# Optimization experiments

Hardware: AMD Instinct MI355X
Metric: run time of the kernel (lower is better)

Reference implementation:

```python
import jax, jax.numpy as jnp
import numpy as np

N_NODES = 50000
N_EDGES = 1_600_000
IN_DIM = 64
HID_DIM = 64
OUT_DIM = 64


def setup_inputs() -> dict:
    key = jax.random.key(0)
    k = jax.random.split(key, 7)
    feat = jax.random.normal(k[0], (N_NODES, IN_DIM), dtype=jnp.float32)
    src = jax.random.randint(k[1], (N_EDGES,), 0, N_NODES, dtype=jnp.int32)
    dst = jax.random.randint(k[2], (N_EDGES,), 0, N_NODES, dtype=jnp.int32)
    # nn.init.normal_(weight, std=0.1); bias default uniform ~ small, use 0.1*randn
    W1 = 0.1 * jax.random.normal(k[3], (HID_DIM, IN_DIM), dtype=jnp.float32)
    b1 = 0.1 * jax.random.normal(k[4], (HID_DIM,), dtype=jnp.float32)
    W2 = 0.1 * jax.random.normal(k[5], (OUT_DIM, HID_DIM), dtype=jnp.float32)
    b2 = 0.1 * jax.random.normal(k[6], (OUT_DIM,), dtype=jnp.float32)
    return {"feat": feat, "src": src, "dst": dst, "W1": W1, "b1": b1, "W2": W2, "b2": b2}


def _gnn_layer(h, src, dst, W, b):
    # copy_u + sum: gather source-node features along edges, scatter-sum to dst
    agg = jax.ops.segment_sum(h[src], dst, num_segments=N_NODES)  # [N, d_in]
    return agg @ W.T + b  # nn.Linear


def reference(feat, src, dst, W1, b1, W2, b2):
    h = _gnn_layer(feat, src, dst, W1, b1)
    h = jnp.tanh(h)
    h = _gnn_layer(h, src, dst, W2, b2)
    return h
```

## Files before the change

### kernel.cpp

```cpp
#include <hip/hip_runtime.h>

#define N_NODES 50000
#define N_EDGES 1600000
#define DIM 64
#define NBK 196
#define BIN_BLOCKS 391
#define CSR_CAP 12288
#define OCT_CAP 1536
#define BCAP 13312
#define G1_BLOCKS 391
#define NB_AGG8 6250

__device__ __forceinline__ unsigned short f2bf(float f) {
    union { float f; unsigned u; } v; v.f = f;
    unsigned r = v.u + 0x7FFF + ((v.u >> 16) & 1);
    return (unsigned short)(r >> 16);
}
__device__ __forceinline__ float bf2f(unsigned short h) {
    union { unsigned u; float f; } v; v.u = ((unsigned)h) << 16;  return v.f;
}
__device__ __forceinline__ float blo(unsigned u) {
    union { unsigned u; float f; } v; v.u = u << 16; return v.f;
}
__device__ __forceinline__ float bhi(unsigned u) {
    union { unsigned u; float f; } v; v.u = u & 0xFFFF0000u; return v.f;
}

__global__ __launch_bounds__(512) void bin_edges(const int* __restrict__ src,
                                                 const int* __restrict__ dst,
                                                 int* __restrict__ bcur,
                                                 int* __restrict__ binned) {
    __shared__ int cnt[256];
    __shared__ int lofs[256];
    __shared__ int shiftv[256];
    __shared__ uint2 stag2[4096];
    int tid = threadIdx.x;

    if (tid < 256) cnt[tid] = 0;
    __syncthreads();

    int base = blockIdx.x * 4096;
    int oct = blockIdx.x & 7;
    int nedge = N_EDGES - base;
    if (nedge > 4096) nedge = 4096;

    int sreg[8], dreg[8];
#pragma unroll
    for (int i = 0; i < 8; ++i) {
        int e = base + i * 512 + tid;
        if (e < N_EDGES) { sreg[i] = src[e]; dreg[i] = dst[e]; }
        else             { sreg[i] = 0;      dreg[i] = -1; }
    }
    int myr[8];
#pragma unroll
    for (int i = 0; i < 8; ++i)
        if (dreg[i] >= 0) myr[i] = atomicAdd(&cnt[dreg[i] >> 8], 1);
    __syncthreads();

    if (tid < 64) {
        int c0 = cnt[tid * 4 + 0];
        int c1 = cnt[tid * 4 + 1];
        int c2 = cnt[tid * 4 + 2];
        int c3 = cnt[tid * 4 + 3];
        int t = c0 + c1 + c2 + c3;
        int p = t;
#pragma unroll
        for (int off = 1; off < 64; off <<= 1) {
            int u = __shfl_up(p, off);
            if (tid >= off) p += u;
        }
        int ex = p - t;
        int b0 = tid * 4;
        lofs[b0 + 0] = ex;
        lofs[b0 + 1] = ex + c0;
        lofs[b0 + 2] = ex + c0 + c1;
        lofs[b0 + 3] = ex + c0 + c1 + c2;
        if (b0 + 0 < NBK && c0) shiftv[b0 + 0] = (b0 + 0) * CSR_CAP + oct * OCT_CAP
            + atomicAdd(&bcur[((b0 + 0) * 8 + oct) * 16], c0) - lofs[b0 + 0];
        if (b0 + 1 < NBK && c1) shiftv[b0 + 1] = (b0 + 1) * CSR_CAP + oct * OCT_CAP
            + atomicAdd(&bcur[((b0 + 1) * 8 + oct) * 16], c1) - lofs[b0 + 1];
        if (b0 + 2 < NBK && c2) shiftv[b0 + 2] = (b0 + 2) * CSR_CAP + oct * OCT_CAP
            + atomicAdd(&bcur[((b0 + 2) * 8 + oct) * 16], c2) - lofs[b0 + 2];
        if (b0 + 3 < NBK && c3) shiftv[b0 + 3] = (b0 + 3) * CSR_CAP + oct * OCT_CAP
            + atomicAdd(&bcur[((b0 + 3) * 8 + oct) * 16], c3) - lofs[b0 + 3];
    }
    __syncthreads();

#pragma unroll
    for (int i = 0; i < 8; ++i) {
        if (dreg[i] >= 0) {
            int b = dreg[i] >> 8;
            uint2 rec;
            rec.x = (unsigned)(((dreg[i] & 255) << 16) | sreg[i]);
            rec.y = (unsigned)b;
            stag2[lofs[b] + myr[i]] = rec;
        }
    }
    __syncthreads();

    for (int i = tid; i < nedge; i += 512) {
        uint2 v = stag2[i];
        binned[i + shiftv[v.y]] = (int)v.x;
    }
}

__global__ __launch_bounds__(256) void csr_gemm1(const int* __restrict__ binned,
                                                 const int* __restrict__ bcur,
                                                 unsigned* __restrict__ nodeinfo,
                                                 unsigned short* __restrict__ csr16,
                                                 const float* __restrict__ X,
                                                 const float* __restrict__ W,
                                                 unsigned short* __restrict__ T) {
    __shared__ __align__(16) char smem[32768];
    int tid = threadIdx.x;

    if (blockIdx.x >= NBK) {
        float4* xs = (float4*)smem;
        int w = tid >> 6, lane = tid & 63;
        int nbase = (blockIdx.x - NBK) * 128;

        float4 wreg[16];
        const float4* wp = (const float4*)(W + lane * 64);
#pragma unroll
        for (int k4 = 0; k4 < 16; ++k4) wreg[k4] = wp[k4];

        const float4* xg = (const float4*)X;
        for (int L = tid; L < 2048; L += 256) {
            int row = nbase + (L >> 4);
            float4 v = {0.f, 0.f, 0.f, 0.f};
            if (row < N_NODES) v = xg[(size_t)row * 16 + (L & 15)];
            xs[L] = v;
        }
        __syncthreads();

        for (int g = 0; g < 8; ++g) {
            int n0 = w * 32 + g * 4;
            float accA = 0.f, accB = 0.f, accC = 0.f, accD = 0.f;
#pragma unroll
            for (int k4 = 0; k4 < 16; ++k4) {
                float4 w4 = wreg[k4];
                float4 xA = xs[(n0 + 0) * 16 + k4];
                float4 xB = xs[(n0 + 1) * 16 + k4];
                float4 xC = xs[(n0 + 2) * 16 + k4];
                float4 xD = xs[(n0 + 3) * 16 + k4];
                accA += xA.x * w4.x + xA.y * w4.y + xA.z * w4.z + xA.w * w4.w;
                accB += xB.x * w4.x + xB.y * w4.y + xB.z * w4.z + xB.w * w4.w;
                accC += xC.x * w4.x + xC.y * w4.y + xC.z * w4.z + xC.w * w4.w;
                accD += xD.x * w4.x + xD.y * w4.y + xD.z * w4.z + xD.w * w4.w;
            }
            int gn = nbase + n0;
            unsigned short vA = (gn + 0 == N_NODES) ? (unsigned short)0 : f2bf(accA);
            unsigned short vB = (gn + 1 == N_NODES) ? (unsigned short)0 : f2bf(accB);
            unsigned short vC = (gn + 2 == N_NODES) ? (unsigned short)0 : f2bf(accC);
            unsigned short vD = (gn + 3 == N_NODES) ? (unsigned short)0 : f2bf(accD);
            if (gn + 0 <= N_NODES) T[(size_t)(gn + 0) * 64 + lane] = vA;
            if (gn + 1 <= N_NODES) T[(size_t)(gn + 1) * 64 + lane] = vB;
            if (gn + 2 <= N_NODES) T[(size_t)(gn + 2) * 64 + lane] = vC;
            if (gn + 3 <= N_NODES) T[(size_t)(gn + 3) * 64 + lane] = vD;
        }
        return;
    }

    int* cnt  = (int*)smem;
    int* cnt2 = cnt + 256;
    int* ofs  = cnt2 + 256;
    int* sb   = ofs + 256;
    int* mo   = sb + 256;
    int b = blockIdx.x;
    int bbase = b * BCAP;
    cnt[tid] = 0; cnt2[tid] = 0;
    if (tid < 8) {
        int m = bcur[(b * 8 + tid) * 16];
        mo[tid] = m > OCT_CAP ? OCT_CAP : m;
    }
    __syncthreads();

    for (int oct = 0; oct < 8; ++oct) {
        const int* ib = binned + b * CSR_CAP + oct * OCT_CAP;
        int m = mo[oct];
        int i = tid;
        for (; i + 768 < m; i += 1024) {
            int p0 = ib[i], p1 = ib[i + 256], p2 = ib[i + 512], p3 = ib[i + 768];
            atomicAdd(&cnt[(p0 >> 16) & 255], 1);
            atomicAdd(&cnt[(p1 >> 16) & 255], 1);
            atomicAdd(&cnt[(p2 >> 16) & 255], 1);
            atomicAdd(&cnt[(p3 >> 16) & 255], 1);
        }
        for (; i < m; i += 256)
            atomicAdd(&cnt[(ib[i] >> 16) & 255], 1);
    }
    __syncthreads();

    int myc = cnt[tid];
    int v = (myc + 15) & ~15;
    sb[tid] = v;
    __syncthreads();
    for (int off = 1; off < 256; off <<= 1) {
        int u = (tid >= off) ? sb[tid - off] : 0;
        __syncthreads();
        sb[tid] += u;
        __syncthreads();
    }
    int o = sb[tid] - v;
    ofs[tid] = o;
    int node = (b << 8) + tid;
    if (node < N_NODES)
        nodeinfo[node] = ((unsigned)v << 23) | (unsigned)(bbase + o);
    for (int i = myc; i < v; ++i)
        csr16[bbase + o + i] = (unsigned short)N_NODES;
    __syncthreads();

    for (int oct = 0; oct < 8; ++oct) {
        const int* ib = binned + b * CSR_CAP + oct * OCT_CAP;
        int m = mo[oct];
        int i = tid;
        for (; i + 768 < m; i += 1024) {
            int p0 = ib[i], p1 = ib[i + 256], p2 = ib[i + 512], p3 = ib[i + 768];
            int d0 = (p0 >> 16) & 255, d1 = (p1 >> 16) & 255;
            int d2 = (p2 >> 16) & 255, d3 = (p3 >> 16) & 255;
            int r0 = atomicAdd(&cnt2[d0], 1);
            int r1 = atomicAdd(&cnt2[d1], 1);
            int r2 = atomicAdd(&cnt2[d2], 1);
            int r3 = atomicAdd(&cnt2[d3], 1);
            csr16[bbase + ofs[d0] + r0] = (unsigned short)(p0 & 0xFFFF);
            csr16[bbase + ofs[d1] + r1] = (unsigned short)(p1 & 0xFFFF);
            csr16[bbase + ofs[d2] + r2] = (unsigned short)(p2 & 0xFFFF);
            csr16[bbase + ofs[d3] + r3] = (unsigned short)(p3 & 0xFFFF);
        }
        for (; i < m; i += 256) {
            int p = ib[i];
            int dl = (p >> 16) & 255;
            int r = atomicAdd(&cnt2[dl], 1);
            csr16[bbase + ofs[dl] + r] = (unsigned short)(p & 0xFFFF);
        }
    }
}

#define ACC8(d)                                                     \
    a0 += blo(d.x); a1 += bhi(d.x); a2 += blo(d.y); a3 += bhi(d.y); \
    a4 += blo(d.z); a5 += bhi(d.z); a6 += blo(d.w); a7 += bhi(d.w);

__global__ __launch_bounds__(512) void agg_fuse1(const unsigned short* __restrict__ T,
                                                 const unsigned short* __restrict__ csr,
                                                 const unsigned* __restrict__ nodeinfo,
                                                 const float* __restrict__ b1,
                                                 const float* __restrict__ W2,
                                                 unsigned short* __restrict__ T2) {
    __shared__ __align__(16) float4 W2t4[1024];
    __shared__ __align__(16) float part[8][8][72];
    int tid = threadIdx.x;
    int w = tid >> 6;
    int lane = tid & 63;
    int g8 = lane >> 3;
    int fs = lane & 7;
    int node = blockIdx.x * 8 + w;

    for (int L4 = tid; L4 < 1024; L4 += 512) {
        int k4 = L4 >> 6, f = L4 & 63;
        W2t4[L4] = *(const float4*)(W2 + f * 64 + k4 * 4);
    }

    unsigned info = nodeinfo[node];
    float bias = b1[lane];
    int pos = (int)(info & 0x7FFFFFu);
    int nch = (int)(info >> 23) >> 3;
    const unsigned short* ip = csr + pos + g8;
    const uint4* Tp = (const uint4*)T;
    float a0 = 0.f, a1 = 0.f, a2 = 0.f, a3 = 0.f, a4 = 0.f, a5 = 0.f, a6 = 0.f, a7 = 0.f;
    int c = 0;
    for (; c + 4 <= nch; c += 4) {
        int j0 = ip[c * 8];
        int j1 = ip[c * 8 + 8];
        int j2 = ip[c * 8 + 16];
        int j3 = ip[c * 8 + 24];
        uint4 d0 = Tp[j0 * 8 + fs];
        uint4 d1 = Tp[j1 * 8 + fs];
        uint4 d2 = Tp[j2 * 8 + fs];
        uint4 d3 = Tp[j3 * 8 + fs];
        ACC8(d0) ACC8(d1) ACC8(d2) ACC8(d3)
    }
    if (c < nch) {
        int j0 = ip[c * 8];
        int j1 = ip[c * 8 + 8];
        uint4 d0 = Tp[j0 * 8 + fs];
        uint4 d1 = Tp[j1 * 8 + fs];
        ACC8(d0) ACC8(d1)
    }
    float4 pa = {a0, a1, a2, a3};
    float4 pb = {a4, a5, a6, a7};
    *(float4*)&part[w][g8][fs * 8] = pa;
    *(float4*)&part[w][g8][fs * 8 + 4] = pb;
    __syncthreads();

    float acc = bias;
#pragma unroll
    for (int g = 0; g < 8; ++g) acc += part[w][g][lane];

    float e = __expf(2.f * acc);
    part[w][0][lane] = 1.f - 2.f / (e + 1.f);

    const float* hrow = &part[w][0][0];
    float tf = 0.f;
#pragma unroll
    for (int k4 = 0; k4 < 16; ++k4) {
        float4 hv = *(const float4*)(hrow + k4 * 4);
        float4 wv = W2t4[k4 * 64 + lane];
        tf += hv.x * wv.x + hv.y * wv.y + hv.z * wv.z + hv.w * wv.w;
    }
    T2[(size_t)node * DIM + lane] = f2bf(tf);

    if (blockIdx.x == 0 && tid < 64)
        T2[(size_t)N_NODES * DIM + tid] = 0;
}

__global__ __launch_bounds__(512) void agg_out(const unsigned short* __restrict__ T,
                                               const unsigned short* __restrict__ csr,
                                               const unsigned* __restrict__ nodeinfo,
                                               const float* __restrict__ bias,
                                               float* __restrict__ outp) {
    __shared__ __align__(16) float part[8][8][72];
    int tid = threadIdx.x;
    int w = tid >> 6;
    int lane = tid & 63;
    int g8 = lane >> 3;
    int fs = lane & 7;
    int node = blockIdx.x * 8 + w;

    unsigned info = nodeinfo[node];
    float bv = bias[lane];
    int pos = (int)(info & 0x7FFFFFu);
    int nch = (int)(info >> 23) >> 3;
    const unsigned short* ip = csr + pos + g8;
    const uint4* Tp = (const uint4*)T;
    float a0 = 0.f, a1 = 0.f, a2 = 0.f, a3 = 0.f, a4 = 0.f, a5 = 0.f, a6 = 0.f, a7 = 0.f;
    int c = 0;
    for (; c + 4 <= nch; c += 4) {
        int j0 = ip[c * 8];
        int j1 = ip[c * 8 + 8];
        int j2 = ip[c * 8 + 16];
        int j3 = ip[c * 8 + 24];
        uint4 d0 = Tp[j0 * 8 + fs];
        uint4 d1 = Tp[j1 * 8 + fs];
        uint4 d2 = Tp[j2 * 8 + fs];
        uint4 d3 = Tp[j3 * 8 + fs];
        ACC8(d0) ACC8(d1) ACC8(d2) ACC8(d3)
    }
    if (c < nch) {
        int j0 = ip[c * 8];
        int j1 = ip[c * 8 + 8];
        uint4 d0 = Tp[j0 * 8 + fs];
        uint4 d1 = Tp[j1 * 8 + fs];
        ACC8(d0) ACC8(d1)
    }
    float4 pa = {a0, a1, a2, a3};
    float4 pb = {a4, a5, a6, a7};
    *(float4*)&part[w][g8][fs * 8] = pa;
    *(float4*)&part[w][g8][fs * 8 + 4] = pb;

    float acc = bv;
#pragma unroll
    for (int g = 0; g < 8; ++g) acc += part[w][g][lane];
    __builtin_nontemporal_store(acc, outp + (size_t)node * DIM + lane);
}

extern "C" void kernel_launch(void* const* d_in, const int* in_sizes, int n_in,
                              void* d_out, int out_size, void* d_ws, size_t ws_size,
                              hipStream_t stream) {
    const float* feat = (const float*)d_in[0];
    const int*   src  = (const int*)d_in[1];
    const int*   dst  = (const int*)d_in[2];
    const float* W1   = (const float*)d_in[3];
    const float* b1   = (const float*)d_in[4];
    const float* W2   = (const float*)d_in[5];
    const float* b2   = (const float*)d_in[6];
    float* out = (float*)d_out;

    int*            binned   = (int*)d_ws;
    unsigned short* csr16    = (unsigned short*)(binned + NBK * CSR_CAP);
    unsigned*       nodeinfo = (unsigned*)(csr16 + NBK * BCAP);
    int*            bcur     = (int*)(nodeinfo + N_NODES);
    unsigned short* t        = (unsigned short*)(bcur + NBK * 8 * 16 + 8);
    unsigned short* t2       = t + (size_t)(N_NODES + 1) * 64;

    (void)hipMemsetAsync(bcur, 0, NBK * 8 * 16 * sizeof(int), stream);
    bin_edges<<<BIN_BLOCKS, 512, 0, stream>>>(src, dst, bcur, binned);
    csr_gemm1<<<NBK + G1_BLOCKS, 256, 0, stream>>>(
        binned, bcur, nodeinfo, csr16, feat, W1, t);

    agg_fuse1<<<NB_AGG8, 512, 0, stream>>>(t, csr16, nodeinfo, b1, W2, t2);

    agg_out<<<NB_AGG8, 512, 0, stream>>>(t2, csr16, nodeinfo, b2, out);
}
```

Before: 203.5 us.

## Split CSR build into per-octant histogram, scan, and scatter kernels

The CSR construction, which ran as 196 blocks each walking eight octants serially, is split into three kernels. A histogram kernel and a scatter kernel each use 1568 blocks, one per bucket-octant pair, and a scan kernel (still fused with the first GEMM) computes per-octant offsets between them. This exposes more parallelism than the 196 serial blocks allowed. The cost is two extra kernel launches and a global histogram buffer that is written and read back.

Result: slower. 210.9 us (+3.6%).

```diff
diff --git a/kernel.cpp b/kernel.cpp
--- a/kernel.cpp
+++ b/kernel.cpp
@@ -9,6 +9,7 @@
 #define OCT_CAP 1536
 #define BCAP 13312
 #define G1_BLOCKS 391
+#define HO_BLOCKS (NBK * 8)
 #define NB_AGG8 6250
 
 __device__ __forceinline__ unsigned short f2bf(float f) {
@@ -104,13 +105,39 @@
     }
 }
 
-__global__ __launch_bounds__(256) void csr_gemm1(const int* __restrict__ binned,
-                                                 const int* __restrict__ bcur,
-                                                 unsigned* __restrict__ nodeinfo,
-                                                 unsigned short* __restrict__ csr16,
-                                                 const float* __restrict__ X,
-                                                 const float* __restrict__ W,
-                                                 unsigned short* __restrict__ T) {
+__global__ __launch_bounds__(256) void hist_oct(const int* __restrict__ binned,
+                                                const int* __restrict__ bcur,
+                                                int* __restrict__ hist) {
+    __shared__ int cnt[256];
+    int tid = threadIdx.x;
+    int b = blockIdx.x >> 3, oct = blockIdx.x & 7;
+    cnt[tid] = 0;
+    __syncthreads();
+
+    int m = bcur[(b * 8 + oct) * 16];
+    if (m > OCT_CAP) m = OCT_CAP;
+    const int* ib = binned + b * CSR_CAP + oct * OCT_CAP;
+    int i = tid;
+    for (; i + 768 < m; i += 1024) {
+        int p0 = ib[i], p1 = ib[i + 256], p2 = ib[i + 512], p3 = ib[i + 768];
+        atomicAdd(&cnt[(p0 >> 16) & 255], 1);
+        atomicAdd(&cnt[(p1 >> 16) & 255], 1);
+        atomicAdd(&cnt[(p2 >> 16) & 255], 1);
+        atomicAdd(&cnt[(p3 >> 16) & 255], 1);
+    }
+    for (; i < m; i += 256)
+        atomicAdd(&cnt[(ib[i] >> 16) & 255], 1);
+    __syncthreads();
+
+    hist[(b * 8 + oct) * 256 + tid] = cnt[tid];
+}
+
+__global__ __launch_bounds__(256) void scan_gemm1(int* __restrict__ hist,
+                                                  unsigned* __restrict__ nodeinfo,
+                                                  unsigned short* __restrict__ csr16,
+                                                  const float* __restrict__ X,
+                                                  const float* __restrict__ W,
+                                                  unsigned short* __restrict__ T) {
     __shared__ __align__(16) char smem[32768];
     int tid = threadIdx.x;
 
@@ -161,38 +188,16 @@
         return;
     }
 
-    int* cnt  = (int*)smem;
-    int* cnt2 = cnt + 256;
-    int* ofs  = cnt2 + 256;
-    int* sb   = ofs + 256;
-    int* mo   = sb + 256;
+    int* sb = (int*)smem;
     int b = blockIdx.x;
     int bbase = b * BCAP;
-    cnt[tid] = 0; cnt2[tid] = 0;
-    if (tid < 8) {
-        int m = bcur[(b * 8 + tid) * 16];
-        mo[tid] = m > OCT_CAP ? OCT_CAP : m;
-    }
-    __syncthreads();
-
-    for (int oct = 0; oct < 8; ++oct) {
-        const int* ib = binned + b * CSR_CAP + oct * OCT_CAP;
-        int m = mo[oct];
-        int i = tid;
-        for (; i + 768 < m; i += 1024) {
-            int p0 = ib[i], p1 = ib[i + 256], p2 = ib[i + 512], p3 = ib[i + 768];
-            atomicAdd(&cnt[(p0 >> 16) & 255], 1);
-            atomicAdd(&cnt[(p1 >> 16) & 255], 1);
-            atomicAdd(&cnt[(p2 >> 16) & 255], 1);
-            atomicAdd(&cnt[(p3 >> 16) & 255], 1);
-        }
-        for (; i < m; i += 256)
-            atomicAdd(&cnt[(ib[i] >> 16) & 255], 1);
-    }
-    __syncthreads();
-
-    int myc = cnt[tid];
-    int v = (myc + 15) & ~15;
+    int* hb = hist + b * 2048;
+
+    int h[8];
+    int tot = 0;
+#pragma unroll
+    for (int oc = 0; oc < 8; ++oc) { h[oc] = hb[oc * 256 + tid]; tot += h[oc]; }
+    int v = (tot + 15) & ~15;
     sb[tid] = v;
     __syncthreads();
     for (int off = 1; off < 256; off <<= 1) {
@@ -202,37 +207,52 @@
         __syncthreads();
     }
     int o = sb[tid] - v;
-    ofs[tid] = o;
     int node = (b << 8) + tid;
     if (node < N_NODES)
         nodeinfo[node] = ((unsigned)v << 23) | (unsigned)(bbase + o);
-    for (int i = myc; i < v; ++i)
+
+    int run = bbase + o;
+#pragma unroll
+    for (int oc = 0; oc < 8; ++oc) { hb[oc * 256 + tid] = run; run += h[oc]; }
+
+    for (int i = tot; i < v; ++i)
         csr16[bbase + o + i] = (unsigned short)N_NODES;
-    __syncthreads();
-
-    for (int oct = 0; oct < 8; ++oct) {
-        const int* ib = binned + b * CSR_CAP + oct * OCT_CAP;
-        int m = mo[oct];
-        int i = tid;
-        for (; i + 768 < m; i += 1024) {
-            int p0 = ib[i], p1 = ib[i + 256], p2 = ib[i + 512], p3 = ib[i + 768];
-            int d0 = (p0 >> 16) & 255, d1 = (p1 >> 16) & 255;
-            int d2 = (p2 >> 16) & 255, d3 = (p3 >> 16) & 255;
-            int r0 = atomicAdd(&cnt2[d0], 1);
-            int r1 = atomicAdd(&cnt2[d1], 1);
-            int r2 = atomicAdd(&cnt2[d2], 1);
-            int r3 = atomicAdd(&cnt2[d3], 1);
-            csr16[bbase + ofs[d0] + r0] = (unsigned short)(p0 & 0xFFFF);
-            csr16[bbase + ofs[d1] + r1] = (unsigned short)(p1 & 0xFFFF);
-            csr16[bbase + ofs[d2] + r2] = (unsigned short)(p2 & 0xFFFF);
-            csr16[bbase + ofs[d3] + r3] = (unsigned short)(p3 & 0xFFFF);
-        }
-        for (; i < m; i += 256) {
-            int p = ib[i];
-            int dl = (p >> 16) & 255;
-            int r = atomicAdd(&cnt2[dl], 1);
-            csr16[bbase + ofs[dl] + r] = (unsigned short)(p & 0xFFFF);
-        }
+}
+
+__global__ __launch_bounds__(256) void scatter_oct(const int* __restrict__ binned,
+                                                   const int* __restrict__ bcur,
+                                                   const int* __restrict__ hist,
+                                                   unsigned short* __restrict__ csr16) {
+    __shared__ int obase[256];
+    __shared__ int cnt[256];
+    int tid = threadIdx.x;
+    int b = blockIdx.x >> 3, oct = blockIdx.x & 7;
+    obase[tid] = hist[(b * 8 + oct) * 256 + tid];
+    cnt[tid] = 0;
+    __syncthreads();
+
+    int m = bcur[(b * 8 + oct) * 16];
+    if (m > OCT_CAP) m = OCT_CAP;
+    const int* ib = binned + b * CSR_CAP + oct * OCT_CAP;
+    int i = tid;
+    for (; i + 768 < m; i += 1024) {
+        int p0 = ib[i], p1 = ib[i + 256], p2 = ib[i + 512], p3 = ib[i + 768];
+        int d0 = (p0 >> 16) & 255, d1 = (p1 >> 16) & 255;
+        int d2 = (p2 >> 16) & 255, d3 = (p3 >> 16) & 255;
+        int r0 = atomicAdd(&cnt[d0], 1);
+        int r1 = atomicAdd(&cnt[d1], 1);
+        int r2 = atomicAdd(&cnt[d2], 1);
+        int r3 = atomicAdd(&cnt[d3], 1);
+        csr16[obase[d0] + r0] = (unsigned short)(p0 & 0xFFFF);
+        csr16[obase[d1] + r1] = (unsigned short)(p1 & 0xFFFF);
+        csr16[obase[d2] + r2] = (unsigned short)(p2 & 0xFFFF);
+        csr16[obase[d3] + r3] = (unsigned short)(p3 & 0xFFFF);
+    }
+    for (; i < m; i += 256) {
+        int p = ib[i];
+        int dl = (p >> 16) & 255;
+        int r = atomicAdd(&cnt[dl], 1);
+        csr16[obase[dl] + r] = (unsigned short)(p & 0xFFFF);
     }
 }
 
@@ -379,13 +399,16 @@
     unsigned short* csr16    = (unsigned short*)(binned + NBK * CSR_CAP);
     unsigned*       nodeinfo = (unsigned*)(csr16 + NBK * BCAP);
     int*            bcur     = (int*)(nodeinfo + N_NODES);
-    unsigned short* t        = (unsigned short*)(bcur + NBK * 8 * 16 + 8);
+    int*            hist     = bcur + NBK * 8 * 16;
+    unsigned short* t        = (unsigned short*)(hist + NBK * 8 * 256 + 8);
     unsigned short* t2       = t + (size_t)(N_NODES + 1) * 64;
 
     (void)hipMemsetAsync(bcur, 0, NBK * 8 * 16 * sizeof(int), stream);
     bin_edges<<<BIN_BLOCKS, 512, 0, stream>>>(src, dst, bcur, binned);
-    csr_gemm1<<<NBK + G1_BLOCKS, 256, 0, stream>>>(
-        binned, bcur, nodeinfo, csr16, feat, W1, t);
+    hist_oct<<<HO_BLOCKS, 256, 0, stream>>>(binned, bcur, hist);
+    scan_gemm1<<<NBK + G1_BLOCKS, 256, 0, stream>>>(
+        hist, nodeinfo, csr16, feat, W1, t);
+    scatter_oct<<<HO_BLOCKS, 256, 0, stream>>>(binned, bcur, hist, csr16);
 
     agg_fuse1<<<NB_AGG8, 512, 0, stream>>>(t, csr16, nodeinfo, b1, W2, t2);
 
```
